# Kernel optimization log

Hardware: AMD Instinct MI355X
Metric: run time of the kernel (lower is better)

## Reference

```python
import jax, jax.numpy as jnp
import numpy as np

B, C, H, W, P_OUT = 8, 256, 96, 96, 256
EPS = 1e-5


def setup_inputs() -> dict:
    key = jax.random.key(0)
    k0, k1, k2 = jax.random.split(key, 3)
    x = jax.random.normal(k0, (B, C, H, W), jnp.float32)
    # ConvOffset2D weight: Conv2d(C, 2C, 3, padding=1, bias=False).
    # Original inits to zero; use small random weights for a non-trivial sampling pattern.
    w_off = jax.random.normal(k1, (2 * C, C, 3, 3), jnp.float32) * 0.01
    gamma = jnp.ones((C,), jnp.float32)
    beta = jnp.zeros((C,), jnp.float32)
    # pointwise Conv2d(C, P_OUT, 1, bias=False), kernel squeezed to (out, in)
    w_pw = jax.random.normal(k2, (P_OUT, C), jnp.float32) * (1.0 / np.sqrt(C))
    return {"x": x, "w_off": w_off, "gamma": gamma, "beta": beta, "w_pw": w_pw}


def _bilinear_sample(maps, coords):
    # maps: (N, Hm, Wm); coords: (N, P, 2) with [..., 0]=row(y), [..., 1]=col(x)
    N, Hm, Wm = maps.shape
    cy = jnp.clip(coords[..., 0], 0.0, Hm - 1)
    cx = jnp.clip(coords[..., 1], 0.0, Wm - 1)
    y0 = jnp.floor(cy)
    x0 = jnp.floor(cx)
    y0i = y0.astype(jnp.int32)
    x0i = x0.astype(jnp.int32)
    y1i = jnp.minimum(y0i + 1, Hm - 1)
    x1i = jnp.minimum(x0i + 1, Wm - 1)
    dy = cy - y0
    dx = cx - x0
    flat = maps.reshape(N, Hm * Wm)

    def g(yi, xi):
        return jnp.take_along_axis(flat, yi * Wm + xi, axis=1)

    v00 = g(y0i, x0i)
    v01 = g(y0i, x1i)
    v10 = g(y1i, x0i)
    v11 = g(y1i, x1i)
    top = v00 + (v01 - v00) * dx
    bot = v10 + (v11 - v10) * dx
    return top + (bot - top) * dy  # (N, P)


def reference(x, w_off, gamma, beta, w_pw):
    b, c, h, w = x.shape
    # fixed_padding(kernel=3, dilation=1) -> pad 1 on each side
    xp = jnp.pad(x, ((0, 0), (0, 0), (1, 1), (1, 1)))
    hp, wp = h + 2, w + 2
    # offset conv: (b, 2c, hp, wp)
    offsets = jax.lax.conv_general_dilated(
        xp, w_off, window_strides=(1, 1), padding=((1, 1), (1, 1)),
        dimension_numbers=("NCHW", "OIHW", "NCHW"))
    # original: view(-1, hp, wp, 2)  (flat-order reshape, channel pairs interleave over width)
    off = offsets.reshape(b * c, hp * wp, 2)
    gy, gx = jnp.meshgrid(jnp.arange(hp, dtype=jnp.float32),
                          jnp.arange(wp, dtype=jnp.float32), indexing="ij")
    grid = jnp.stack([gy.ravel(), gx.ravel()], axis=-1)  # (hp*wp, 2)
    coords = off + grid[None]
    sampled = _bilinear_sample(xp.reshape(b * c, hp, wp), coords)
    xd = sampled.reshape(b, c, hp, wp)[:, :, 1:-1, 1:-1]  # crop back to (h, w)
    # BatchNorm2d (training-mode batch statistics, biased var, eps=1e-5)
    mean = jnp.mean(xd, axis=(0, 2, 3), keepdims=True)
    var = jnp.var(xd, axis=(0, 2, 3), keepdims=True)
    xn = (xd - mean) * jax.lax.rsqrt(var + EPS)
    xn = xn * gamma[None, :, None, None] + beta[None, :, None, None]
    xr = jax.nn.relu(xn)
    # pointwise 1x1 conv
    return jnp.einsum("bchw,oc->bohw", xr, w_pw)
```

## Files before the change

### kernel.cpp

```cpp
#include <hip/hip_runtime.h>
#include <hip/hip_bf16.h>
#include <stdint.h>


#define BB 8
#define CI 256
#define HH 96
#define WW 96
#define WP 98
#define NSP 9604
#define NIN 9216
#define OC2 512

typedef __attribute__((ext_vector_type(8))) short short8;
typedef __attribute__((ext_vector_type(4))) float float4v;
typedef __attribute__((ext_vector_type(16))) float float16v;

__device__ __forceinline__ int bf16_mode(const void* gamma) {
  return *(const uint32_t*)gamma == 0x3F803F80u;
}
__device__ __forceinline__ float ldin(const void* p, long i, int bf) {
  return bf ? __bfloat162float(((const __hip_bfloat16*)p)[i])
            : ((const float*)p)[i];
}
__device__ __forceinline__ unsigned short f32_to_bf16_bits(float f) {
  uint32_t u = __float_as_uint(f);
  return (unsigned short)((u + 0x7FFFu + ((u >> 16) & 1u)) >> 16);
}
__device__ __forceinline__ float bf16_bits_to_f32(unsigned short b) {
  return __uint_as_float(((uint32_t)b) << 16);
}
__device__ __forceinline__ unsigned short ldbf(const void* p, long i, int bf) {
  if (bf) return ((const unsigned short*)p)[i];
  return f32_to_bf16_bits(((const float*)p)[i]);
}
__device__ __forceinline__ void gld16(const void* g, void* l) {
  __builtin_amdgcn_global_load_lds(
      (const __attribute__((address_space(1))) unsigned int*)g,
      (__attribute__((address_space(3))) unsigned int*)l, 16, 0, 0);
}

__global__ __launch_bounds__(256) void prep_kernel(
    const void* __restrict__ xin, const void* __restrict__ w_off,
    const void* __restrict__ w_pw, const void* __restrict__ gamma,
    unsigned short* __restrict__ Xp2, unsigned short* __restrict__ Wt,
    unsigned short* __restrict__ Wp) {
  const int bf = bf16_mode(gamma);
  if (blockIdx.x < 10000) {
    const int id = blockIdx.x * 256 + threadIdx.x;
    const int cc = id % 100;
    const int t1 = id / 100;
    const int rr = t1 % 100;
    const int bg = t1 / 100;
    const int y = rr - 2, x = cc - 2;
    const bool inb = ((unsigned)y < 96u) && ((unsigned)x < 96u);
    const long base = ((long)(bg * 8)) * (HH * WW) + (long)y * WW + x;
    short8 o;
#pragma unroll
    for (int j = 0; j < 8; ++j)
      o[j] = inb ? (short)ldbf(xin, base + (long)j * (HH * WW), bf) : (short)0;
    *(short8*)(Xp2 + (long)id * 8) = o;
  } else if (blockIdx.x < 10576) {
    const int id = (blockIdx.x - 10000) * 256 + threadIdx.x;
    const int oc = id & 511;
    const int tg = id >> 9;
    const int g = tg & 31, t = tg >> 5;
    short8 o;
#pragma unroll
    for (int j = 0; j < 8; ++j)
      o[j] = (short)ldbf(w_off, ((long)oc * CI + g * 8 + j) * 9 + t, bf);
    *(short8*)(Wt + (long)id * 8) = o;
  } else {
    const int id = (blockIdx.x - 10576) * 256 + threadIdx.x;
    const int oc = id & 255;
    const int g  = id >> 8;
    short8 o;
#pragma unroll
    for (int j = 0; j < 8; ++j)
      o[j] = (short)ldbf(w_pw, (long)oc * CI + g * 8 + j, bf);
    *(short8*)(Wp + (long)id * 8) = o;
  }
}

#define CONV_PHASE(KK, PF, W)                                                 \
  do {                                                                        \
    short8 af0, af1, bv0, bv1, bv2, bv3, bv4;                                 \
    {                                                                         \
      const int kg = (KK) * 2 + lh;                                           \
      const unsigned short* ap = Ac + (kg * 256 + aRow) * 8;                  \
      af0 = *(const short8*)ap;                                               \
      af1 = *(const short8*)(ap + 256);                                       \
      const unsigned short* bp = Bc + (kg * 320 + bRow) * 8;                  \
      bv0 = *(const short8*)bp;                                               \
      bv1 = *(const short8*)(bp + 256);                                       \
      bv2 = *(const short8*)(bp + 512);                                       \
      bv3 = *(const short8*)(bp + 768);                                       \
      bv4 = *(const short8*)(bp + 1024);                                      \
    }                                                                         \
    PF;                                                                       \
    asm volatile(W ::: "memory");                                             \
    __builtin_amdgcn_s_barrier();                                             \
    __builtin_amdgcn_s_setprio(1);                                            \
    acc[0][0] = __builtin_amdgcn_mfma_f32_32x32x16_bf16(af0, bv0, acc[0][0], 0, 0, 0); \
    acc[0][1] = __builtin_amdgcn_mfma_f32_32x32x16_bf16(af0, bv1, acc[0][1], 0, 0, 0); \
    acc[0][2] = __builtin_amdgcn_mfma_f32_32x32x16_bf16(af0, bv2, acc[0][2], 0, 0, 0); \
    acc[0][3] = __builtin_amdgcn_mfma_f32_32x32x16_bf16(af0, bv3, acc[0][3], 0, 0, 0); \
    acc[0][4] = __builtin_amdgcn_mfma_f32_32x32x16_bf16(af0, bv4, acc[0][4], 0, 0, 0); \
    acc[1][0] = __builtin_amdgcn_mfma_f32_32x32x16_bf16(af1, bv0, acc[1][0], 0, 0, 0); \
    acc[1][1] = __builtin_amdgcn_mfma_f32_32x32x16_bf16(af1, bv1, acc[1][1], 0, 0, 0); \
    acc[1][2] = __builtin_amdgcn_mfma_f32_32x32x16_bf16(af1, bv2, acc[1][2], 0, 0, 0); \
    acc[1][3] = __builtin_amdgcn_mfma_f32_32x32x16_bf16(af1, bv3, acc[1][3], 0, 0, 0); \
    acc[1][4] = __builtin_amdgcn_mfma_f32_32x32x16_bf16(af1, bv4, acc[1][4], 0, 0, 0); \
    __builtin_amdgcn_s_setprio(0);                                            \
    __builtin_amdgcn_s_barrier();                                             \
  } while (0)

__global__ __launch_bounds__(512, 2) void conv_mfma(
    const unsigned short* __restrict__ Xp2, const unsigned short* __restrict__ Wt,
    unsigned short* __restrict__ offp) {
  extern __shared__ __align__(16) unsigned short lds[];
  unsigned short* As0 = lds;
  unsigned short* Bs0 = lds + 32768;

  const int tid = threadIdx.x;
  const int wv = tid >> 6, ln = tid & 63;
  const int lh = ln >> 5, lm = ln & 31;
  const int wm = wv >> 1, wn = wv & 1;
  const int b      = blockIdx.x;
  const int p_blk  = blockIdx.y * 320;
  const int oc_blk = blockIdx.z * 256;

  const int aRow = wm * 64 + lm;
  const int bRow = wn * 160 + lm;

  int aoff[4], boff[5];
#pragma unroll
  for (int j = 0; j < 4; ++j) {
    int id = j * 512 + tid;
    aoff[j] = ((id >> 8) * OC2 + oc_blk + (id & 255)) * 8;
  }
#pragma unroll
  for (int j = 0; j < 5; ++j) {
    int id = j * 512 + tid;
    int kg = id / 320, pl = id - kg * 320;
    int p = p_blk + pl;
    int r = p / WP; if (r > 97) r = 97;
    int c = p - r * WP; if (c > 97) c = 97;
    boff[j] = (kg * 10000 + r * 100 + c) * 8;
  }

  float16v acc[2][5];
#pragma unroll
  for (int m = 0; m < 2; ++m)
#pragma unroll
    for (int n = 0; n < 5; ++n)
#pragma unroll
      for (int r = 0; r < 16; ++r) acc[m][n][r] = 0.f;

  {
    const unsigned short* a2 = Wt;
    const unsigned short* b2 = Xp2 + (size_t)(b * 32) * 10000 * 8;
    gld16(a2 + aoff[0], As0 + (0 * 512 + tid) * 8);
    gld16(b2 + boff[0], Bs0 + (0 * 512 + tid) * 8);
    gld16(b2 + boff[1], Bs0 + (1 * 512 + tid) * 8);
    gld16(a2 + aoff[1], As0 + (1 * 512 + tid) * 8);
    gld16(b2 + boff[2], Bs0 + (2 * 512 + tid) * 8);
    gld16(a2 + aoff[2], As0 + (2 * 512 + tid) * 8);
    gld16(b2 + boff[3], Bs0 + (3 * 512 + tid) * 8);
    gld16(a2 + aoff[3], As0 + (3 * 512 + tid) * 8);
    gld16(b2 + boff[4], Bs0 + (4 * 512 + tid) * 8);
  }
  asm volatile("s_waitcnt vmcnt(6)" ::: "memory");
  __builtin_amdgcn_s_barrier();

  int t2 = 0, icb2 = 0;
  for (int s = 0; s < 35; ++s) {
    if (++t2 == 9) { t2 = 0; ++icb2; }
    const unsigned short* a2 = Wt + (size_t)(t2 * 32 + icb2 * 8) * (OC2 * 8);
    const unsigned short* b2 =
        Xp2 + ((size_t)(b * 32 + icb2 * 8) * 10000 + (t2 / 3) * 100 + (t2 % 3)) * 8;
    const unsigned short* Ac = As0 + (s & 1) * 16384;
    const unsigned short* Bc = Bs0 + (s & 1) * 20480;
    unsigned short* An = As0 + ((s & 1) ^ 1) * 16384;
    unsigned short* Bn = Bs0 + ((s & 1) ^ 1) * 20480;

    CONV_PHASE(0,
        { gld16(a2 + aoff[0], An + (0 * 512 + tid) * 8);
          gld16(b2 + boff[0], Bn + (0 * 512 + tid) * 8); },
        "s_waitcnt vmcnt(6)");
    CONV_PHASE(1,
        { gld16(b2 + boff[1], Bn + (1 * 512 + tid) * 8);
          gld16(a2 + aoff[1], An + (1 * 512 + tid) * 8); },
        "s_waitcnt vmcnt(6)");
    CONV_PHASE(2,
        { gld16(b2 + boff[2], Bn + (2 * 512 + tid) * 8);
          gld16(a2 + aoff[2], An + (2 * 512 + tid) * 8); },
        "s_waitcnt vmcnt(6)");
    CONV_PHASE(3,
        { gld16(b2 + boff[3], Bn + (3 * 512 + tid) * 8);
          gld16(a2 + aoff[3], An + (3 * 512 + tid) * 8);
          gld16(b2 + boff[4], Bn + (4 * 512 + tid) * 8); },
        "s_waitcnt vmcnt(6)");
  }
  {
    const unsigned short* Ac = As0 + 16384;
    const unsigned short* Bc = Bs0 + 20480;
    CONV_PHASE(0, {}, "s_waitcnt vmcnt(4)");
    CONV_PHASE(1, {}, "s_waitcnt vmcnt(2)");
    CONV_PHASE(2, {}, "s_waitcnt vmcnt(0)");
    CONV_PHASE(3, {}, "");
  }

#pragma unroll
  for (int n = 0; n < 5; ++n) {
    const int p = p_blk + wn * 160 + n * 32 + lm;
    if (p < NSP) {
#pragma unroll
      for (int m = 0; m < 2; ++m) {
        const int oc0 = oc_blk + wm * 64 + m * 32 + 4 * lh;
#pragma unroll
        for (int reg = 0; reg < 16; ++reg) {
          const int oc = oc0 + (reg & 3) + 8 * (reg >> 2);
          offp[((long)(b * OC2 + oc)) * NSP + p] = f32_to_bf16_bits(acc[m][n][reg]);
        }
      }
    }
  }
}

__global__ __launch_bounds__(256) void sample_kernel(
    const void* __restrict__ xin, const void* __restrict__ gamma,
    const unsigned short* __restrict__ offp,
    unsigned short* __restrict__ xd, float* __restrict__ partials) {
  const int bf  = bf16_mode(gamma);
  const int tid = threadIdx.x;
  const int n = blockIdx.x;
  const int b = n >> 8, c = n & 255;

  __shared__ __align__(16) unsigned short smap[9608];
  __shared__ float red[8];

  for (int i = tid; i < 1201; i += 256) ((short8*)smap)[i] = (short8)0;
  __syncthreads();
  const long xb = ((long)(b * CI + c)) * (HH * WW);
  for (int q = tid; q < 1152; q += 256) {
    int rr  = q / 12;
    int cc8 = (q - rr * 12) * 8;
    short8 v;
    if (bf) {
      v = *(const short8*)((const unsigned short*)xin + xb + rr * WW + cc8);
    } else {
#pragma unroll
      for (int k = 0; k < 8; ++k)
        v[k] = (short)f32_to_bf16_bits(((const float*)xin)[xb + rr * WW + cc8 + k]);
    }
    int basei = (rr + 1) * WP + 1 + cc8;
#pragma unroll
    for (int k = 0; k < 8; ++k) smap[basei + k] = (unsigned short)v[k];
  }
  __syncthreads();

  const long ob_even = ((long)(b * OC2 + 2 * c)) * NSP;
  const long ob_odd  = ob_even + NSP;
  float s1 = 0.f, s2 = 0.f;

  for (int it = 0; it < 36; ++it) {
    int i = tid + it * 256;
    int r  = 1 + i / WW;
    int cl = 1 + (i - (r - 1) * WW);
    int p  = r * WP + cl;
    long base = (p < 4802) ? (ob_even + 2 * p) : (ob_odd + 2 * (p - 4802));
    uint32_t pair = *(const uint32_t*)(offp + base);
    float offy = bf16_bits_to_f32((unsigned short)(pair & 0xffffu));
    float offx = bf16_bits_to_f32((unsigned short)(pair >> 16));
    float cy = fminf(fmaxf(offy + (float)r, 0.f), 97.f);
    float cx = fminf(fmaxf(offx + (float)cl, 0.f), 97.f);
    float y0 = floorf(cy), x0 = floorf(cx);
    int y0i = (int)y0, x0i = (int)x0;
    int y1i = y0i + 1 < 97 ? y0i + 1 : 97;
    int x1i = x0i + 1 < 97 ? x0i + 1 : 97;
    float dy = cy - y0, dx = cx - x0;
    float v00 = bf16_bits_to_f32(smap[y0i * WP + x0i]);
    float v01 = bf16_bits_to_f32(smap[y0i * WP + x1i]);
    float v10 = bf16_bits_to_f32(smap[y1i * WP + x0i]);
    float v11 = bf16_bits_to_f32(smap[y1i * WP + x1i]);
    float top = v00 + (v01 - v00) * dx;
    float bot = v10 + (v11 - v10) * dx;
    float val = top + (bot - top) * dy;
    unsigned short vb = f32_to_bf16_bits(val);
    float vr = bf16_bits_to_f32(vb);
    xd[(long)n * NIN + i] = vb;
    s1 += vr;
    s2 += vr * vr;
  }

#pragma unroll
  for (int o = 32; o > 0; o >>= 1) {
    s1 += __shfl_down(s1, o, 64);
    s2 += __shfl_down(s2, o, 64);
  }
  if ((tid & 63) == 0) { red[tid >> 6] = s1; red[4 + (tid >> 6)] = s2; }
  __syncthreads();
  if (tid == 0) {
    partials[n]        = red[0] + red[1] + red[2] + red[3];
    partials[2048 + n] = red[4] + red[5] + red[6] + red[7];
  }
}

__global__ __launch_bounds__(256) void bnrelu_t(
    const unsigned short* __restrict__ xd, const float* __restrict__ partials,
    const void* __restrict__ gamma, const void* __restrict__ beta,
    unsigned short* __restrict__ y) {
  const int bf = bf16_mode(gamma);
  const int tid = threadIdx.x;
  const int i0 = blockIdx.x * 64;
  const int b  = blockIdx.y;
  __shared__ unsigned short yt[64 * 256];

  float s1 = 0.f, s2 = 0.f;
#pragma unroll
  for (int bb = 0; bb < BB; ++bb) {
    s1 += partials[bb * 256 + tid];
    s2 += partials[2048 + bb * 256 + tid];
  }
  const float invn = 1.f / (float)(BB * NIN);
  float mean = s1 * invn;
  float var  = s2 * invn - mean * mean;
  float g  = ldin(gamma, tid, bf);
  float be = ldin(beta, tid, bf);
  float sc = g * rsqrtf(var + 1e-5f);
  float sh = be - mean * sc;

  const long xbase = ((long)(b * CI + tid)) * NIN + i0;
#pragma unroll
  for (int j = 0; j < 8; ++j) {
    short8 v = *(const short8*)(xd + xbase + j * 8);
#pragma unroll
    for (int k = 0; k < 8; ++k) {
      float f = bf16_bits_to_f32((unsigned short)v[k]);
      f = fmaxf(fmaf(f, sc, sh), 0.f);
      yt[(j * 8 + k) * 256 + tid] = f32_to_bf16_bits(f);
    }
  }
  __syncthreads();
  const int cb = (tid & 31) * 8;
  const int r0 = tid >> 5;
#pragma unroll
  for (int pass = 0; pass < 8; ++pass) {
    int ii = pass * 8 + r0;
    *(short8*)(y + ((long)(b * NIN + i0 + ii)) * CI + cb) =
        *(const short8*)&yt[ii * 256 + cb];
  }
}

__global__ __launch_bounds__(256) void pw_mfma(
    const unsigned short* __restrict__ y, const unsigned short* __restrict__ Wp,
    const void* __restrict__ gamma, void* __restrict__ out) {
  const int bfo = bf16_mode(gamma);
  __shared__ __align__(16) unsigned short As[8 * 128 * 8];
  __shared__ __align__(16) unsigned short Bs[8 * 128 * 8];
  const int tid = threadIdx.x;
  const int wv = tid >> 6, ln = tid & 63;
  const int b      = blockIdx.x;
  const int p_blk  = blockIdx.y * 128;
  const int oc_blk = blockIdx.z * 128;

  int aoffv[4], boffv[4];
  unsigned short* alds[4];
  unsigned short* blds[4];
#pragma unroll
  for (int i = 0; i < 4; ++i) {
    int id = tid + 256 * i;
    int gl = id >> 7, low = id & 127;
    aoffv[i] = (gl * 256 + oc_blk + low) * 8;
    boffv[i] = (p_blk + low) * CI + gl * 8;
    alds[i] = &As[id * 8];
    blds[i] = &Bs[id * 8];
  }
  const unsigned short* ybase = y + (long)b * NIN * CI;

  float4v acc[4][4];
#pragma unroll
  for (int m = 0; m < 4; ++m)
#pragma unroll
    for (int n = 0; n < 4; ++n) {
      acc[m][n][0] = 0.f; acc[m][n][1] = 0.f;
      acc[m][n][2] = 0.f; acc[m][n][3] = 0.f;
    }

  const int q = ln >> 4, col = ln & 15;
  const int ocw_l = (wv >> 1) * 64;
  const int pw_l  = (wv & 1) * 64;

  for (int ks = 0; ks < 4; ++ks) {
    const unsigned short* astep = Wp + ks * 16384;
    const unsigned short* bstep = ybase + ks * 64;
    __syncthreads();
#pragma unroll
    for (int i = 0; i < 4; ++i) {
      gld16(astep + aoffv[i], alds[i]);
      gld16(bstep + boffv[i], blds[i]);
    }
    __syncthreads();

#pragma unroll
    for (int kk = 0; kk < 2; ++kk) {
      const int qq = kk * 4 + q;
      short8 af[4], bfr[4];
#pragma unroll
      for (int m = 0; m < 4; ++m)
        af[m] = *(const short8*)&As[(qq * 128 + ocw_l + m * 16 + col) * 8];
#pragma unroll
      for (int n = 0; n < 4; ++n)
        bfr[n] = *(const short8*)&Bs[(qq * 128 + pw_l + n * 16 + col) * 8];
#pragma unroll
      for (int m = 0; m < 4; ++m)
#pragma unroll
        for (int n = 0; n < 4; ++n)
          acc[m][n] = __builtin_amdgcn_mfma_f32_16x16x32_bf16(
              af[m], bfr[n], acc[m][n], 0, 0, 0);
    }
  }

#pragma unroll
  for (int m = 0; m < 4; ++m) {
    const int oc = oc_blk + ocw_l + m * 16 + q * 4;
#pragma unroll
    for (int n = 0; n < 4; ++n) {
      const int p = p_blk + pw_l + n * 16 + col;
#pragma unroll
      for (int reg = 0; reg < 4; ++reg) {
        long idx = ((long)(b * CI + oc + reg)) * NIN + p;
        if (bfo) ((__hip_bfloat16*)out)[idx] = __float2bfloat16(acc[m][n][reg]);
        else ((float*)out)[idx] = acc[m][n][reg];
      }
    }
  }
}

extern "C" void kernel_launch(void* const* d_in, const int* in_sizes, int n_in,
                              void* d_out, int out_size, void* d_ws, size_t ws_size,
                              hipStream_t stream) {
  const void* x     = d_in[0];
  const void* w_off = d_in[1];
  const void* gamma = d_in[2];
  const void* beta  = d_in[3];
  const void* w_pw  = d_in[4];

  char*  ws   = (char*)d_ws;
  float* fws  = (float*)ws;
  char*  R1   = ws + 32768;
  unsigned short* Xp2 = (unsigned short*)R1;
  unsigned short* xd  = (unsigned short*)R1;
  unsigned short* yb  = (unsigned short*)(R1 + 37748736);
  unsigned short* Wt  = (unsigned short*)(R1 + 50331648);
  unsigned short* offp = (unsigned short*)(ws + 32768 + 75497472);
  unsigned short* Wp   = (unsigned short*)(ws + 32768 + 75497472 + 78675968);

  static int conv_lds_set = 0;
  if (!conv_lds_set) {
    (void)hipFuncSetAttribute((const void*)conv_mfma,
                              hipFuncAttributeMaxDynamicSharedMemorySize,
                              147456);
    conv_lds_set = 1;
  }

  prep_kernel<<<dim3(10608), 256, 0, stream>>>(x, w_off, w_pw, gamma, Xp2, Wt, Wp);
  conv_mfma<<<dim3(BB, 31, 2), dim3(512), 147456, stream>>>(Xp2, Wt, offp);
  sample_kernel<<<dim3(2048), 256, 0, stream>>>(x, gamma, offp, xd, fws);
  bnrelu_t<<<dim3(144, BB), 256, 0, stream>>>(xd, fws, gamma, beta, yb);
  pw_mfma<<<dim3(BB, 72, 2), 256, 0, stream>>>(yb, Wp, gamma, d_out);
}
```

Baseline: 403.4 us.

## Load conv weight fragments directly to registers, drop LDS staging for A

The offset-conv MFMA kernel no longer stages the weight (A) tile through LDS. Each wave loads its A fragments straight from global memory into registers, double-buffered as even/odd pairs and prefetched one phase ahead. Only the activation (B) tile stays in LDS, so dynamic LDS drops from 147456 to 81920 bytes, and three of the four per-phase trailing barriers are removed. The cost is redundant global/L2 reads of weights across waves, plus more delicate vmcnt accounting that could stall or race.

Result: slower. 428.1 us (+6.1%).

```diff
diff --git a/kernel.cpp b/kernel.cpp
--- a/kernel.cpp
+++ b/kernel.cpp
@@ -82,45 +82,44 @@
   }
 }
 
-#define CONV_PHASE(KK, PF, W)                                                 \
+#define ALOAD(D0, D1, BASE, KG)                                               \
+  { const short8* lap_ = (const short8*)((BASE) + ((size_t)(KG)*OC2 + aocb)*8); \
+    D0 = lap_[0]; D1 = lap_[32]; }
+
+#define CONV_PHASE(KK, AU0, AU1, AL0, AL1, LKG, LBASE, PFB, W, BAR2)          \
   do {                                                                        \
-    short8 af0, af1, bv0, bv1, bv2, bv3, bv4;                                 \
-    {                                                                         \
-      const int kg = (KK) * 2 + lh;                                           \
-      const unsigned short* ap = Ac + (kg * 256 + aRow) * 8;                  \
-      af0 = *(const short8*)ap;                                               \
-      af1 = *(const short8*)(ap + 256);                                       \
-      const unsigned short* bp = Bc + (kg * 320 + bRow) * 8;                  \
-      bv0 = *(const short8*)bp;                                               \
-      bv1 = *(const short8*)(bp + 256);                                       \
-      bv2 = *(const short8*)(bp + 512);                                       \
-      bv3 = *(const short8*)(bp + 768);                                       \
-      bv4 = *(const short8*)(bp + 1024);                                      \
-    }                                                                         \
-    PF;                                                                       \
+    PFB;                                                                      \
+    ALOAD(AL0, AL1, LBASE, LKG);                                              \
+    short8 bv0, bv1, bv2, bv3, bv4;                                           \
+    { const int kg_ = (KK) * 2 + lh;                                          \
+      const unsigned short* bp_ = Bc + (kg_ * 320 + bRow) * 8;                \
+      bv0 = *(const short8*)bp_;                                              \
+      bv1 = *(const short8*)(bp_ + 256);                                      \
+      bv2 = *(const short8*)(bp_ + 512);                                      \
+      bv3 = *(const short8*)(bp_ + 768);                                      \
+      bv4 = *(const short8*)(bp_ + 1024); }                                   \
     asm volatile(W ::: "memory");                                             \
     __builtin_amdgcn_s_barrier();                                             \
     __builtin_amdgcn_s_setprio(1);                                            \
-    acc[0][0] = __builtin_amdgcn_mfma_f32_32x32x16_bf16(af0, bv0, acc[0][0], 0, 0, 0); \
-    acc[0][1] = __builtin_amdgcn_mfma_f32_32x32x16_bf16(af0, bv1, acc[0][1], 0, 0, 0); \
-    acc[0][2] = __builtin_amdgcn_mfma_f32_32x32x16_bf16(af0, bv2, acc[0][2], 0, 0, 0); \
-    acc[0][3] = __builtin_amdgcn_mfma_f32_32x32x16_bf16(af0, bv3, acc[0][3], 0, 0, 0); \
-    acc[0][4] = __builtin_amdgcn_mfma_f32_32x32x16_bf16(af0, bv4, acc[0][4], 0, 0, 0); \
-    acc[1][0] = __builtin_amdgcn_mfma_f32_32x32x16_bf16(af1, bv0, acc[1][0], 0, 0, 0); \
-    acc[1][1] = __builtin_amdgcn_mfma_f32_32x32x16_bf16(af1, bv1, acc[1][1], 0, 0, 0); \
-    acc[1][2] = __builtin_amdgcn_mfma_f32_32x32x16_bf16(af1, bv2, acc[1][2], 0, 0, 0); \
-    acc[1][3] = __builtin_amdgcn_mfma_f32_32x32x16_bf16(af1, bv3, acc[1][3], 0, 0, 0); \
-    acc[1][4] = __builtin_amdgcn_mfma_f32_32x32x16_bf16(af1, bv4, acc[1][4], 0, 0, 0); \
+    acc[0][0] = __builtin_amdgcn_mfma_f32_32x32x16_bf16(AU0, bv0, acc[0][0], 0, 0, 0); \
+    acc[0][1] = __builtin_amdgcn_mfma_f32_32x32x16_bf16(AU0, bv1, acc[0][1], 0, 0, 0); \
+    acc[0][2] = __builtin_amdgcn_mfma_f32_32x32x16_bf16(AU0, bv2, acc[0][2], 0, 0, 0); \
+    acc[0][3] = __builtin_amdgcn_mfma_f32_32x32x16_bf16(AU0, bv3, acc[0][3], 0, 0, 0); \
+    acc[0][4] = __builtin_amdgcn_mfma_f32_32x32x16_bf16(AU0, bv4, acc[0][4], 0, 0, 0); \
+    acc[1][0] = __builtin_amdgcn_mfma_f32_32x32x16_bf16(AU1, bv0, acc[1][0], 0, 0, 0); \
+    acc[1][1] = __builtin_amdgcn_mfma_f32_32x32x16_bf16(AU1, bv1, acc[1][1], 0, 0, 0); \
+    acc[1][2] = __builtin_amdgcn_mfma_f32_32x32x16_bf16(AU1, bv2, acc[1][2], 0, 0, 0); \
+    acc[1][3] = __builtin_amdgcn_mfma_f32_32x32x16_bf16(AU1, bv3, acc[1][3], 0, 0, 0); \
+    acc[1][4] = __builtin_amdgcn_mfma_f32_32x32x16_bf16(AU1, bv4, acc[1][4], 0, 0, 0); \
     __builtin_amdgcn_s_setprio(0);                                            \
-    __builtin_amdgcn_s_barrier();                                             \
+    BAR2;                                                                     \
   } while (0)
 
 __global__ __launch_bounds__(512, 2) void conv_mfma(
     const unsigned short* __restrict__ Xp2, const unsigned short* __restrict__ Wt,
     unsigned short* __restrict__ offp) {
   extern __shared__ __align__(16) unsigned short lds[];
-  unsigned short* As0 = lds;
-  unsigned short* Bs0 = lds + 32768;
+  unsigned short* Bs0 = lds;
 
   const int tid = threadIdx.x;
   const int wv = tid >> 6, ln = tid & 63;
@@ -130,15 +129,10 @@
   const int p_blk  = blockIdx.y * 320;
   const int oc_blk = blockIdx.z * 256;
 
-  const int aRow = wm * 64 + lm;
+  const int aocb = oc_blk + wm * 64 + lm;
   const int bRow = wn * 160 + lm;
 
-  int aoff[4], boff[5];
-#pragma unroll
-  for (int j = 0; j < 4; ++j) {
-    int id = j * 512 + tid;
-    aoff[j] = ((id >> 8) * OC2 + oc_blk + (id & 255)) * 8;
-  }
+  int boff[5];
 #pragma unroll
   for (int j = 0; j < 5; ++j) {
     int id = j * 512 + tid;
@@ -157,58 +151,49 @@
 #pragma unroll
       for (int r = 0; r < 16; ++r) acc[m][n][r] = 0.f;
 
+  short8 afE0, afE1, afO0, afO1;
+  const unsigned short* acur = Wt;
+
+  ALOAD(afE0, afE1, Wt, lh);
   {
-    const unsigned short* a2 = Wt;
     const unsigned short* b2 = Xp2 + (size_t)(b * 32) * 10000 * 8;
-    gld16(a2 + aoff[0], As0 + (0 * 512 + tid) * 8);
-    gld16(b2 + boff[0], Bs0 + (0 * 512 + tid) * 8);
-    gld16(b2 + boff[1], Bs0 + (1 * 512 + tid) * 8);
-    gld16(a2 + aoff[1], As0 + (1 * 512 + tid) * 8);
-    gld16(b2 + boff[2], Bs0 + (2 * 512 + tid) * 8);
-    gld16(a2 + aoff[2], As0 + (2 * 512 + tid) * 8);
-    gld16(b2 + boff[3], Bs0 + (3 * 512 + tid) * 8);
-    gld16(a2 + aoff[3], As0 + (3 * 512 + tid) * 8);
-    gld16(b2 + boff[4], Bs0 + (4 * 512 + tid) * 8);
-  }
-  asm volatile("s_waitcnt vmcnt(6)" ::: "memory");
+#pragma unroll
+    for (int j = 0; j < 5; ++j)
+      gld16(b2 + boff[j], Bs0 + (j * 512 + tid) * 8);
+  }
+  asm volatile("s_waitcnt vmcnt(0)" ::: "memory");
   __builtin_amdgcn_s_barrier();
 
   int t2 = 0, icb2 = 0;
   for (int s = 0; s < 35; ++s) {
     if (++t2 == 9) { t2 = 0; ++icb2; }
-    const unsigned short* a2 = Wt + (size_t)(t2 * 32 + icb2 * 8) * (OC2 * 8);
+    const unsigned short* anext = Wt + (size_t)(t2 * 32 + icb2 * 8) * (OC2 * 8);
     const unsigned short* b2 =
         Xp2 + ((size_t)(b * 32 + icb2 * 8) * 10000 + (t2 / 3) * 100 + (t2 % 3)) * 8;
-    const unsigned short* Ac = As0 + (s & 1) * 16384;
     const unsigned short* Bc = Bs0 + (s & 1) * 20480;
-    unsigned short* An = As0 + ((s & 1) ^ 1) * 16384;
     unsigned short* Bn = Bs0 + ((s & 1) ^ 1) * 20480;
 
-    CONV_PHASE(0,
-        { gld16(a2 + aoff[0], An + (0 * 512 + tid) * 8);
-          gld16(b2 + boff[0], Bn + (0 * 512 + tid) * 8); },
-        "s_waitcnt vmcnt(6)");
-    CONV_PHASE(1,
-        { gld16(b2 + boff[1], Bn + (1 * 512 + tid) * 8);
-          gld16(a2 + aoff[1], An + (1 * 512 + tid) * 8); },
-        "s_waitcnt vmcnt(6)");
-    CONV_PHASE(2,
-        { gld16(b2 + boff[2], Bn + (2 * 512 + tid) * 8);
-          gld16(a2 + aoff[2], An + (2 * 512 + tid) * 8); },
-        "s_waitcnt vmcnt(6)");
-    CONV_PHASE(3,
-        { gld16(b2 + boff[3], Bn + (3 * 512 + tid) * 8);
-          gld16(a2 + aoff[3], An + (3 * 512 + tid) * 8);
-          gld16(b2 + boff[4], Bn + (4 * 512 + tid) * 8); },
-        "s_waitcnt vmcnt(6)");
+    CONV_PHASE(0, afE0, afE1, afO0, afO1, 2 + lh, acur,
+               { gld16(b2 + boff[0], Bn + (0 * 512 + tid) * 8); },
+               "s_waitcnt vmcnt(7)", ((void)0));
+    CONV_PHASE(1, afO0, afO1, afE0, afE1, 4 + lh, acur,
+               { gld16(b2 + boff[1], Bn + (1 * 512 + tid) * 8); },
+               "s_waitcnt vmcnt(7)", ((void)0));
+    CONV_PHASE(2, afE0, afE1, afO0, afO1, 6 + lh, acur,
+               { gld16(b2 + boff[2], Bn + (2 * 512 + tid) * 8); },
+               "s_waitcnt vmcnt(9)", ((void)0));
+    CONV_PHASE(3, afO0, afO1, afE0, afE1, 0 + lh, anext,
+               { gld16(b2 + boff[3], Bn + (3 * 512 + tid) * 8);
+                 gld16(b2 + boff[4], Bn + (4 * 512 + tid) * 8); },
+               "s_waitcnt vmcnt(7)", __builtin_amdgcn_s_barrier());
+    acur = anext;
   }
   {
-    const unsigned short* Ac = As0 + 16384;
     const unsigned short* Bc = Bs0 + 20480;
-    CONV_PHASE(0, {}, "s_waitcnt vmcnt(4)");
-    CONV_PHASE(1, {}, "s_waitcnt vmcnt(2)");
-    CONV_PHASE(2, {}, "s_waitcnt vmcnt(0)");
-    CONV_PHASE(3, {}, "");
+    CONV_PHASE(0, afE0, afE1, afO0, afO1, 2 + lh, acur, {}, "s_waitcnt vmcnt(6)", ((void)0));
+    CONV_PHASE(1, afO0, afO1, afE0, afE1, 4 + lh, acur, {}, "s_waitcnt vmcnt(5)", ((void)0));
+    CONV_PHASE(2, afE0, afE1, afO0, afO1, 6 + lh, acur, {}, "s_waitcnt vmcnt(6)", ((void)0));
+    CONV_PHASE(3, afO0, afO1, afE0, afE1, 0 + lh, acur, {}, "", ((void)0));
   }
 
 #pragma unroll
@@ -461,12 +446,12 @@
   if (!conv_lds_set) {
     (void)hipFuncSetAttribute((const void*)conv_mfma,
                               hipFuncAttributeMaxDynamicSharedMemorySize,
-                              147456);
+                              81920);
     conv_lds_set = 1;
   }
 
   prep_kernel<<<dim3(10608), 256, 0, stream>>>(x, w_off, w_pw, gamma, Xp2, Wt, Wp);
-  conv_mfma<<<dim3(BB, 31, 2), dim3(512), 147456, stream>>>(Xp2, Wt, offp);
+  conv_mfma<<<dim3(BB, 31, 2), dim3(512), 81920, stream>>>(Xp2, Wt, offp);
   sample_kernel<<<dim3(2048), 256, 0, stream>>>(x, gamma, offp, xd, fws);
   bnrelu_t<<<dim3(144, BB), 256, 0, stream>>>(xd, fws, gamma, beta, yb);
   pw_mfma<<<dim3(BB, 72, 2), 256, 0, stream>>>(yb, Wp, gamma, d_out);
```

## Drop conv mid-phase barriers and widen pointwise GEMM tile to all outputs

Applied to the files above, without the earlier changes.

In the offset-conv MFMA loop, the second s_barrier of each phase is removed except after phase 3, and sched_barrier fences are added so the compiler cannot move work across the barriers. The pointwise 1x1 GEMM kernel now computes all 256 output channels per block instead of 128, which halves the grid and loads each activation tile once instead of twice. The costs are doubled accumulator registers and larger LDS per block in the pointwise kernel. Removing the barriers relies on double-buffer ordering to prevent LDS races.

Result: slower. 421.4 us (+4.5%).

```diff
diff --git a/kernel.cpp b/kernel.cpp
--- a/kernel.cpp
+++ b/kernel.cpp
@@ -82,7 +82,7 @@
   }
 }
 
-#define CONV_PHASE(KK, PF, W)                                                 \
+#define CONV_PHASE(KK, PF, W, BAR2)                                           \
   do {                                                                        \
     short8 af0, af1, bv0, bv1, bv2, bv3, bv4;                                 \
     {                                                                         \
@@ -100,6 +100,7 @@
     PF;                                                                       \
     asm volatile(W ::: "memory");                                             \
     __builtin_amdgcn_s_barrier();                                             \
+    __builtin_amdgcn_sched_barrier(0);                                        \
     __builtin_amdgcn_s_setprio(1);                                            \
     acc[0][0] = __builtin_amdgcn_mfma_f32_32x32x16_bf16(af0, bv0, acc[0][0], 0, 0, 0); \
     acc[0][1] = __builtin_amdgcn_mfma_f32_32x32x16_bf16(af0, bv1, acc[0][1], 0, 0, 0); \
@@ -112,8 +113,10 @@
     acc[1][3] = __builtin_amdgcn_mfma_f32_32x32x16_bf16(af1, bv3, acc[1][3], 0, 0, 0); \
     acc[1][4] = __builtin_amdgcn_mfma_f32_32x32x16_bf16(af1, bv4, acc[1][4], 0, 0, 0); \
     __builtin_amdgcn_s_setprio(0);                                            \
-    __builtin_amdgcn_s_barrier();                                             \
+    BAR2;                                                                     \
   } while (0)
+
+#define CONV_BAR2 { __builtin_amdgcn_s_barrier(); __builtin_amdgcn_sched_barrier(0); }
 
 __global__ __launch_bounds__(512, 2) void conv_mfma(
     const unsigned short* __restrict__ Xp2, const unsigned short* __restrict__ Wt,
@@ -133,11 +136,11 @@
   const int aRow = wm * 64 + lm;
   const int bRow = wn * 160 + lm;
 
-  int aoff[4], boff[5];
+  int aoffv[4], boff[5];
 #pragma unroll
   for (int j = 0; j < 4; ++j) {
     int id = j * 512 + tid;
-    aoff[j] = ((id >> 8) * OC2 + oc_blk + (id & 255)) * 8;
+    aoffv[j] = ((id >> 8) * OC2 + oc_blk + (id & 255)) * 8;
   }
 #pragma unroll
   for (int j = 0; j < 5; ++j) {
@@ -160,18 +163,19 @@
   {
     const unsigned short* a2 = Wt;
     const unsigned short* b2 = Xp2 + (size_t)(b * 32) * 10000 * 8;
-    gld16(a2 + aoff[0], As0 + (0 * 512 + tid) * 8);
+    gld16(a2 + aoffv[0], As0 + (0 * 512 + tid) * 8);
     gld16(b2 + boff[0], Bs0 + (0 * 512 + tid) * 8);
     gld16(b2 + boff[1], Bs0 + (1 * 512 + tid) * 8);
-    gld16(a2 + aoff[1], As0 + (1 * 512 + tid) * 8);
+    gld16(a2 + aoffv[1], As0 + (1 * 512 + tid) * 8);
     gld16(b2 + boff[2], Bs0 + (2 * 512 + tid) * 8);
-    gld16(a2 + aoff[2], As0 + (2 * 512 + tid) * 8);
+    gld16(a2 + aoffv[2], As0 + (2 * 512 + tid) * 8);
     gld16(b2 + boff[3], Bs0 + (3 * 512 + tid) * 8);
-    gld16(a2 + aoff[3], As0 + (3 * 512 + tid) * 8);
+    gld16(a2 + aoffv[3], As0 + (3 * 512 + tid) * 8);
     gld16(b2 + boff[4], Bs0 + (4 * 512 + tid) * 8);
   }
   asm volatile("s_waitcnt vmcnt(6)" ::: "memory");
   __builtin_amdgcn_s_barrier();
+  __builtin_amdgcn_sched_barrier(0);
 
   int t2 = 0, icb2 = 0;
   for (int s = 0; s < 35; ++s) {
@@ -185,30 +189,30 @@
     unsigned short* Bn = Bs0 + ((s & 1) ^ 1) * 20480;
 
     CONV_PHASE(0,
-        { gld16(a2 + aoff[0], An + (0 * 512 + tid) * 8);
+        { gld16(a2 + aoffv[0], An + (0 * 512 + tid) * 8);
           gld16(b2 + boff[0], Bn + (0 * 512 + tid) * 8); },
-        "s_waitcnt vmcnt(6)");
+        "s_waitcnt vmcnt(6)", ((void)0));
     CONV_PHASE(1,
         { gld16(b2 + boff[1], Bn + (1 * 512 + tid) * 8);
-          gld16(a2 + aoff[1], An + (1 * 512 + tid) * 8); },
-        "s_waitcnt vmcnt(6)");
+          gld16(a2 + aoffv[1], An + (1 * 512 + tid) * 8); },
+        "s_waitcnt vmcnt(6)", ((void)0));
     CONV_PHASE(2,
         { gld16(b2 + boff[2], Bn + (2 * 512 + tid) * 8);
-          gld16(a2 + aoff[2], An + (2 * 512 + tid) * 8); },
-        "s_waitcnt vmcnt(6)");
+          gld16(a2 + aoffv[2], An + (2 * 512 + tid) * 8); },
+        "s_waitcnt vmcnt(6)", ((void)0));
     CONV_PHASE(3,
         { gld16(b2 + boff[3], Bn + (3 * 512 + tid) * 8);
-          gld16(a2 + aoff[3], An + (3 * 512 + tid) * 8);
+          gld16(a2 + aoffv[3], An + (3 * 512 + tid) * 8);
           gld16(b2 + boff[4], Bn + (4 * 512 + tid) * 8); },
-        "s_waitcnt vmcnt(6)");
+        "s_waitcnt vmcnt(6)", CONV_BAR2);
   }
   {
     const unsigned short* Ac = As0 + 16384;
     const unsigned short* Bc = Bs0 + 20480;
-    CONV_PHASE(0, {}, "s_waitcnt vmcnt(4)");
-    CONV_PHASE(1, {}, "s_waitcnt vmcnt(2)");
-    CONV_PHASE(2, {}, "s_waitcnt vmcnt(0)");
-    CONV_PHASE(3, {}, "");
+    CONV_PHASE(0, {}, "s_waitcnt vmcnt(4)", ((void)0));
+    CONV_PHASE(1, {}, "s_waitcnt vmcnt(2)", ((void)0));
+    CONV_PHASE(2, {}, "s_waitcnt vmcnt(0)", ((void)0));
+    CONV_PHASE(3, {}, "", ((void)0));
   }
 
 #pragma unroll
@@ -357,36 +361,41 @@
     const unsigned short* __restrict__ y, const unsigned short* __restrict__ Wp,
     const void* __restrict__ gamma, void* __restrict__ out) {
   const int bfo = bf16_mode(gamma);
-  __shared__ __align__(16) unsigned short As[8 * 128 * 8];
+  __shared__ __align__(16) unsigned short As[8 * 256 * 8];
   __shared__ __align__(16) unsigned short Bs[8 * 128 * 8];
   const int tid = threadIdx.x;
   const int wv = tid >> 6, ln = tid & 63;
   const int b      = blockIdx.x;
   const int p_blk  = blockIdx.y * 128;
-  const int oc_blk = blockIdx.z * 128;
-
-  int aoffv[4], boffv[4];
-  unsigned short* alds[4];
+
+  int aoffv[8], boffv[4];
+  unsigned short* alds[8];
   unsigned short* blds[4];
+#pragma unroll
+  for (int i = 0; i < 8; ++i) {
+    int id = tid + 256 * i;
+    aoffv[i] = id * 8;
+    alds[i] = &As[id * 8];
+  }
 #pragma unroll
   for (int i = 0; i < 4; ++i) {
     int id = tid + 256 * i;
     int gl = id >> 7, low = id & 127;
-    aoffv[i] = (gl * 256 + oc_blk + low) * 8;
     boffv[i] = (p_blk + low) * CI + gl * 8;
-    alds[i] = &As[id * 8];
     blds[i] = &Bs[id * 8];
   }
   const unsigned short* ybase = y + (long)b * NIN * CI;
 
-  float4v acc[4][4];
-#pragma unroll
-  for (int m = 0; m < 4; ++m)
-#pragma unroll
-    for (int n = 0; n < 4; ++n) {
-      acc[m][n][0] = 0.f; acc[m][n][1] = 0.f;
-      acc[m][n][2] = 0.f; acc[m][n][3] = 0.f;
-    }
+  float4v acc[2][4][4];
+#pragma unroll
+  for (int oh = 0; oh < 2; ++oh)
+#pragma unroll
+    for (int m = 0; m < 4; ++m)
+#pragma unroll
+      for (int n = 0; n < 4; ++n) {
+        acc[oh][m][n][0] = 0.f; acc[oh][m][n][1] = 0.f;
+        acc[oh][m][n][2] = 0.f; acc[oh][m][n][3] = 0.f;
+      }
 
   const int q = ln >> 4, col = ln & 15;
   const int ocw_l = (wv >> 1) * 64;
@@ -397,45 +406,50 @@
     const unsigned short* bstep = ybase + ks * 64;
     __syncthreads();
 #pragma unroll
-    for (int i = 0; i < 4; ++i) {
-      gld16(astep + aoffv[i], alds[i]);
-      gld16(bstep + boffv[i], blds[i]);
-    }
+    for (int i = 0; i < 8; ++i) gld16(astep + aoffv[i], alds[i]);
+#pragma unroll
+    for (int i = 0; i < 4; ++i) gld16(bstep + boffv[i], blds[i]);
     __syncthreads();
 
 #pragma unroll
     for (int kk = 0; kk < 2; ++kk) {
       const int qq = kk * 4 + q;
-      short8 af[4], bfr[4];
-#pragma unroll
-      for (int m = 0; m < 4; ++m)
-        af[m] = *(const short8*)&As[(qq * 128 + ocw_l + m * 16 + col) * 8];
+      short8 bfr[4];
 #pragma unroll
       for (int n = 0; n < 4; ++n)
         bfr[n] = *(const short8*)&Bs[(qq * 128 + pw_l + n * 16 + col) * 8];
 #pragma unroll
-      for (int m = 0; m < 4; ++m)
-#pragma unroll
-        for (int n = 0; n < 4; ++n)
-          acc[m][n] = __builtin_amdgcn_mfma_f32_16x16x32_bf16(
-              af[m], bfr[n], acc[m][n], 0, 0, 0);
-    }
-  }
-
-#pragma unroll
-  for (int m = 0; m < 4; ++m) {
-    const int oc = oc_blk + ocw_l + m * 16 + q * 4;
-#pragma unroll
-    for (int n = 0; n < 4; ++n) {
-      const int p = p_blk + pw_l + n * 16 + col;
-#pragma unroll
-      for (int reg = 0; reg < 4; ++reg) {
-        long idx = ((long)(b * CI + oc + reg)) * NIN + p;
-        if (bfo) ((__hip_bfloat16*)out)[idx] = __float2bfloat16(acc[m][n][reg]);
-        else ((float*)out)[idx] = acc[m][n][reg];
+      for (int oh = 0; oh < 2; ++oh) {
+        short8 af[4];
+#pragma unroll
+        for (int m = 0; m < 4; ++m)
+          af[m] = *(const short8*)&As[(qq * 256 + oh * 128 + ocw_l + m * 16 + col) * 8];
+#pragma unroll
+        for (int m = 0; m < 4; ++m)
+#pragma unroll
+          for (int n = 0; n < 4; ++n)
+            acc[oh][m][n] = __builtin_amdgcn_mfma_f32_16x16x32_bf16(
+                af[m], bfr[n], acc[oh][m][n], 0, 0, 0);
       }
     }
   }
+
+#pragma unroll
+  for (int oh = 0; oh < 2; ++oh)
+#pragma unroll
+    for (int m = 0; m < 4; ++m) {
+      const int oc = oh * 128 + ocw_l + m * 16 + q * 4;
+#pragma unroll
+      for (int n = 0; n < 4; ++n) {
+        const int p = p_blk + pw_l + n * 16 + col;
+#pragma unroll
+        for (int reg = 0; reg < 4; ++reg) {
+          long idx = ((long)(b * CI + oc + reg)) * NIN + p;
+          if (bfo) ((__hip_bfloat16*)out)[idx] = __float2bfloat16(acc[oh][m][n][reg]);
+          else ((float*)out)[idx] = acc[oh][m][n][reg];
+        }
+      }
+    }
 }
 
 extern "C" void kernel_launch(void* const* d_in, const int* in_sizes, int n_in,
@@ -469,5 +483,5 @@
   conv_mfma<<<dim3(BB, 31, 2), dim3(512), 147456, stream>>>(Xp2, Wt, offp);
   sample_kernel<<<dim3(2048), 256, 0, stream>>>(x, gamma, offp, xd, fws);
   bnrelu_t<<<dim3(144, BB), 256, 0, stream>>>(xd, fws, gamma, beta, yb);
-  pw_mfma<<<dim3(BB, 72, 2), 256, 0, stream>>>(yb, Wp, gamma, d_out);
-}
+  pw_mfma<<<dim3(BB, 72), 256, 0, stream>>>(yb, Wp, gamma, d_out);
+}
```
